# Performance work log

Hardware: AMD Instinct MI355X
Metric: run time of the kernel (lower is better)

Reference implementation:

```python
import jax, jax.numpy as jnp
import numpy as np
from jax import lax

K = 3  # kernel size
KK = K * K


def _bilinear_gather(img, ys, xs):
    """img: [C, H, W]; ys, xs: [KK, H, W] float sample coords.
    Returns [C, KK, H, W], zero outside the image (torch DCN zero-pad semantics)."""
    C, H, W = img.shape
    y0 = jnp.floor(ys).astype(jnp.int32)
    x0 = jnp.floor(xs).astype(jnp.int32)
    y1, x1 = y0 + 1, x0 + 1
    wy1 = ys - y0.astype(ys.dtype)
    wx1 = xs - x0.astype(xs.dtype)
    wy0, wx0 = 1.0 - wy1, 1.0 - wx1

    def g(yi, xi):
        valid = ((yi >= 0) & (yi < H) & (xi >= 0) & (xi < W)).astype(img.dtype)
        yc = jnp.clip(yi, 0, H - 1)
        xc = jnp.clip(xi, 0, W - 1)
        return img[:, yc, xc] * valid[None]  # [C, KK, H, W]

    return (wy0 * wx0) * g(y0, x0) + (wy0 * wx1) * g(y0, x1) \
         + (wy1 * wx0) * g(y1, x0) + (wy1 * wx1) * g(y1, x1)


def _df_layer(x, w_off, b_off, w):
    """One DFConv2d (modulated DCN, k=3, s=1, d=1, pad=1, groups=1) + ReLU."""
    B, C, H, W = x.shape
    O = w.shape[0]
    # offset/mask conv (standard 3x3, pad 1, with bias)
    om = lax.conv_general_dilated(x, w_off, (1, 1), [(1, 1), (1, 1)],
                                  dimension_numbers=('NCHW', 'OIHW', 'NCHW'))
    om = om + b_off[None, :, None, None]                     # [B, 27, H, W]
    off = om[:, :2 * KK].reshape(B, KK, 2, H, W)             # (dy, dx) per kernel pt
    mask = jax.nn.sigmoid(om[:, 2 * KK:3 * KK])              # [B, KK, H, W]

    ki, kj = jnp.meshgrid(jnp.arange(K), jnp.arange(K), indexing='ij')
    # base sampling grid: y = h - pad + i*dil = h + i - 1
    base_y = jnp.arange(H, dtype=x.dtype)[None, :, None] + (ki.reshape(KK, 1, 1).astype(x.dtype) - 1.0)
    base_x = jnp.arange(W, dtype=x.dtype)[None, None, :] + (kj.reshape(KK, 1, 1).astype(x.dtype) - 1.0)
    ys = base_y + off[:, :, 0]                               # [B, KK, H, W]
    xs = base_x + off[:, :, 1]

    sampled = jax.vmap(_bilinear_gather)(x, ys, xs)          # [B, C, KK, H, W]
    out = jnp.einsum('oik,bikhw->bohw', w.reshape(O, C, KK), sampled * mask[:, None])
    return jax.nn.relu(out)


def setup_inputs() -> dict:
    key = jax.random.key(0)
    ks = jax.random.split(key, 7)
    s = 0.05
    return {
        'x': jax.random.normal(ks[0], (2, 256, 96, 96), dtype=jnp.float32),
        'w_off0': jax.random.normal(ks[1], (27, 256, 3, 3), dtype=jnp.float32) * s,
        'b_off0': jnp.zeros((27,), dtype=jnp.float32),
        'w0': jax.random.normal(ks[2], (256, 256, 3, 3), dtype=jnp.float32) * s,
        'w_off1': jax.random.normal(ks[3], (27, 256, 3, 3), dtype=jnp.float32) * s,
        'b_off1': jnp.zeros((27,), dtype=jnp.float32),
        'w1': jax.random.normal(ks[4], (256, 256, 3, 3), dtype=jnp.float32) * s,
    }


def reference(x, w_off0, b_off0, w0, w_off1, b_off1, w1):
    h = _df_layer(x, w_off0, b_off0, w0)
    h = _df_layer(h, w_off1, b_off1, w1)
    return h
```

## Files before the change

### kernel.cpp

```cpp
#include <hip/hip_runtime.h>
#include <cstdint>
#include <cstddef>


#define KTOT 2304
#define PXB  9216

typedef __attribute__((ext_vector_type(8))) short bf16x8;
typedef __attribute__((ext_vector_type(4))) float f32x4;

static __device__ __forceinline__ unsigned short f2bf(float f) {
    union { float f; unsigned int u; } v; v.f = f;
    unsigned int r = (v.u + 0x7FFFu + ((v.u >> 16) & 1u)) >> 16;
    return (unsigned short)r;
}
static __device__ __forceinline__ float bf2f(unsigned short h) {
    union { unsigned int u; float f; } v; v.u = ((unsigned int)h) << 16;
    return v.f;
}
static __device__ __forceinline__ void unpack8(uint4 u, float* f) {
    union { unsigned int u; float f; } t;
    t.u = u.x << 16;         f[0] = t.f;
    t.u = u.x & 0xffff0000u; f[1] = t.f;
    t.u = u.y << 16;         f[2] = t.f;
    t.u = u.y & 0xffff0000u; f[3] = t.f;
    t.u = u.z << 16;         f[4] = t.f;
    t.u = u.z & 0xffff0000u; f[5] = t.f;
    t.u = u.w << 16;         f[6] = t.f;
    t.u = u.w & 0xffff0000u; f[7] = t.f;
}

__global__ __launch_bounds__(256) void transpose_kernel(const float* __restrict__ in,
                                                        unsigned short* __restrict__ outH,
                                                        unsigned short* __restrict__ outL) {
    __shared__ float tile[64][65];
    const int hw0 = blockIdx.x * 64;
    const int c0  = blockIdx.y * 64;
    const int b   = blockIdx.z;
    const int lx  = threadIdx.x & 63;
    const int ly  = threadIdx.x >> 6;
#pragma unroll
    for (int i = 0; i < 16; ++i) {
        int cl = ly + i * 4;
        tile[cl][lx] = in[(size_t)(b * 256 + c0 + cl) * PXB + hw0 + lx];
    }
    __syncthreads();
#pragma unroll
    for (int i = 0; i < 16; ++i) {
        int hwl = ly + i * 4;
        float v = tile[lx][hwl];
        size_t oi = ((size_t)b * PXB + hw0 + hwl) * 256 + c0 + lx;
        unsigned short hi = f2bf(v);
        outH[oi] = hi;
        outL[oi] = f2bf(v - bf2f(hi));
    }
}

__global__ __launch_bounds__(256) void prep_w_kernel(const float* __restrict__ w,
                                                     unsigned short* __restrict__ wA) {
    int idx = blockIdx.x * 256 + threadIdx.x;
    int o = idx / KTOT;
    int k = idx - o * KTOT;
    int kk = k >> 8;
    int c  = k & 255;
    wA[idx] = f2bf(w[o * KTOT + c * 9 + kk]);
}

__global__ __launch_bounds__(256) void prep_woff_kernel(const float* __restrict__ w,
                                                        unsigned short* __restrict__ wH,
                                                        unsigned short* __restrict__ wL) {
    int idx = blockIdx.x * 256 + threadIdx.x;
    int o = idx / KTOT;
    int k = idx - o * KTOT;
    int kk = k >> 8;
    int c  = k & 255;
    float f = (o < 27) ? w[o * KTOT + c * 9 + kk] : 0.0f;
    unsigned short hi = f2bf(f);
    wH[idx] = hi;
    wL[idx] = f2bf(f - bf2f(hi));
}

__global__ __launch_bounds__(512) void offconv_fused(const unsigned short* __restrict__ xH,
                                                     const unsigned short* __restrict__ xL,
                                                     const unsigned short* __restrict__ AH,
                                                     const unsigned short* __restrict__ AL,
                                                     const float* __restrict__ bias,
                                                     float* __restrict__ om) {
    __shared__ __attribute__((aligned(16))) unsigned short AsH[2][32 * 72];
    __shared__ __attribute__((aligned(16))) unsigned short AsL[2][32 * 72];
    __shared__ __attribute__((aligned(16))) unsigned short BsH[2][64 * 72];
    __shared__ __attribute__((aligned(16))) unsigned short BsL[2][64 * 72];

    const int tid  = threadIdx.x;
    const int kg   = tid >> 8;
    const int tl   = tid & 255;
    const int lane = tid & 63;
    const int wq   = (tid >> 6) & 3;
    const int quad = lane >> 4, l16 = lane & 15;
    const int g    = blockIdx.x;
    const int nb   = (g & 7) * 36 + (g >> 3);
    const int n0   = nb * 64;
    const int b    = n0 / PXB;
    const int hw0  = n0 - b * PXB;

    f32x4 acc[2];
#pragma unroll
    for (int mt = 0; mt < 2; ++mt) acc[mt] = (f32x4)0.0f;

    const int arow = tl >> 3, akg = tl & 7;

    uint4 pAH, pAL, pBH0, pBL0, pBH1, pBL1;
    auto pf = [&](int it) {
        const int kt = kg * 18 + it;
        const int kk = kt >> 2, c0 = (kt & 3) * 64;
        const int dy = kk / 3 - 1, dx = kk - (kk / 3) * 3 - 1;
        size_t ai = (size_t)arow * KTOT + kt * 64 + akg * 8;
        pAH = *(const uint4*)&AH[ai];
        pAL = *(const uint4*)&AL[ai];
#pragma unroll
        for (int i = 0; i < 2; ++i) {
            int task = i * 256 + tl;
            int px = task >> 3, cg = task & 7;
            int hw = hw0 + px;
            int h = hw / 96, w = hw - h * 96;
            int y = h + dy, x = w + dx;
            uint4 hv = make_uint4(0u, 0u, 0u, 0u), lv = make_uint4(0u, 0u, 0u, 0u);
            if (((unsigned)y < 96u) && ((unsigned)x < 96u)) {
                size_t bi = ((size_t)b * PXB + y * 96 + x) * 256 + c0 + cg * 8;
                hv = *(const uint4*)&xH[bi];
                lv = *(const uint4*)&xL[bi];
            }
            if (i == 0) { pBH0 = hv; pBL0 = lv; } else { pBH1 = hv; pBL1 = lv; }
        }
    };
    pf(0);

    for (int it = 0; it < 18; ++it) {
        __syncthreads();
        *(uint4*)&AsH[kg][arow * 72 + akg * 8] = pAH;
        *(uint4*)&AsL[kg][arow * 72 + akg * 8] = pAL;
        {
            int px = tl >> 3, cg = tl & 7;
            *(uint4*)&BsH[kg][px * 72 + cg * 8] = pBH0;
            *(uint4*)&BsL[kg][px * 72 + cg * 8] = pBL0;
        }
        {
            int task = 256 + tl;
            int px = task >> 3, cg = task & 7;
            *(uint4*)&BsH[kg][px * 72 + cg * 8] = pBH1;
            *(uint4*)&BsL[kg][px * 72 + cg * 8] = pBL1;
        }
        if (it < 17) pf(it + 1);
        __syncthreads();
#pragma unroll
        for (int ks = 0; ks < 2; ++ks) {
            bf16x8 ah[2], al[2], bh, bl;
#pragma unroll
            for (int mt = 0; mt < 2; ++mt) {
                ah[mt] = *(const bf16x8*)&AsH[kg][(mt * 16 + l16) * 72 + ks * 32 + quad * 8];
                al[mt] = *(const bf16x8*)&AsL[kg][(mt * 16 + l16) * 72 + ks * 32 + quad * 8];
            }
            bh = *(const bf16x8*)&BsH[kg][(wq * 16 + l16) * 72 + ks * 32 + quad * 8];
            bl = *(const bf16x8*)&BsL[kg][(wq * 16 + l16) * 72 + ks * 32 + quad * 8];
#pragma unroll
            for (int mt = 0; mt < 2; ++mt) {
                acc[mt] = __builtin_amdgcn_mfma_f32_16x16x32_bf16(ah[mt], bh, acc[mt], 0, 0, 0);
                acc[mt] = __builtin_amdgcn_mfma_f32_16x16x32_bf16(ah[mt], bl, acc[mt], 0, 0, 0);
                acc[mt] = __builtin_amdgcn_mfma_f32_16x16x32_bf16(al[mt], bh, acc[mt], 0, 0, 0);
            }
        }
    }

    float* red = (float*)BsH;
    __syncthreads();
    if (kg == 1) {
#pragma unroll
        for (int mt = 0; mt < 2; ++mt)
#pragma unroll
            for (int r = 0; r < 4; ++r)
                red[wq * 512 + mt * 256 + quad * 64 + r * 16 + l16] = acc[mt][r];
    }
    __syncthreads();
    if (kg == 0) {
#pragma unroll
        for (int mt = 0; mt < 2; ++mt)
#pragma unroll
            for (int r = 0; r < 4; ++r) {
                float v = acc[mt][r] + red[wq * 512 + mt * 256 + quad * 64 + r * 16 + l16];
                int m = mt * 16 + quad * 4 + r;
                int n = wq * 16 + l16;
                if (m < 27)
                    om[(size_t)(b * 27 + m) * PXB + hw0 + n] = v + bias[m];
            }
    }
}

__global__ __launch_bounds__(512) void dfconv_v6(const unsigned short* __restrict__ xB,
                                                 const float* __restrict__ om,
                                                 const unsigned short* __restrict__ A,
                                                 float* __restrict__ out,
                                                 unsigned short* __restrict__ outH,
                                                 unsigned short* __restrict__ outL,
                                                 int out_mode) {
    __shared__ __attribute__((aligned(16))) char smem[104128];
    unsigned short* BsD  = (unsigned short*)(smem + 65536);
    unsigned short* goff = (unsigned short*)(smem + 88576);
    float*          gwt  = (float*)(smem + 93760);

    const int tid  = threadIdx.x;
    const int wv   = tid >> 6;
    const int lane = tid & 63;
    const int quad = lane >> 4, l16 = lane & 15;
    const int g    = blockIdx.x;
    const int nb   = (g & 7) * 32 + (g >> 3);
    const int b    = nb >> 7;
    const int hw0  = (nb & 127) * 72;

    for (int task = tid; task < 648; task += 512) {
        int px = task / 9;
        int kk = task - px * 9;
        int hw = hw0 + px;
        int h = hw / 96, w = hw - h * 96;
        const float* omp = om + (size_t)b * 27 * PXB + hw;
        float dyv = omp[(size_t)(2 * kk) * PXB];
        float dxv = omp[(size_t)(2 * kk + 1) * PXB];
        float mv  = omp[(size_t)(18 + kk) * PXB];
        float mk  = 1.0f / (1.0f + __expf(-mv));

        float ys = (float)(h + (kk / 3) - 1) + dyv;
        float xs = (float)(w + (kk - (kk / 3) * 3) - 1) + dxv;
        float fy = floorf(ys), fx = floorf(xs);
        int iy = (int)fy, ix = (int)fx;
        float wy1 = ys - fy, wx1 = xs - fx;
        float wy0 = 1.0f - wy1, wx0 = 1.0f - wx1;
        bool yv0 = (unsigned)iy < 96u, yv1 = (unsigned)(iy + 1) < 96u;
        bool xv0 = (unsigned)ix < 96u, xv1 = (unsigned)(ix + 1) < 96u;
        int y0 = min(max(iy, 0), 95),     y1 = min(max(iy + 1, 0), 95);
        int x0 = min(max(ix, 0), 95),     x1 = min(max(ix + 1, 0), 95);
        int gg = task * 4;
        goff[gg + 0] = (unsigned short)(y0 * 96 + x0);
        goff[gg + 1] = (unsigned short)(y0 * 96 + x1);
        goff[gg + 2] = (unsigned short)(y1 * 96 + x0);
        goff[gg + 3] = (unsigned short)(y1 * 96 + x1);
        gwt[gg + 0] = (yv0 && xv0) ? mk * wy0 * wx0 : 0.0f;
        gwt[gg + 1] = (yv0 && xv1) ? mk * wy0 * wx1 : 0.0f;
        gwt[gg + 2] = (yv1 && xv0) ? mk * wy1 * wx0 : 0.0f;
        gwt[gg + 3] = (yv1 && xv1) ? mk * wy1 * wx1 : 0.0f;
    }
    for (int i = tid; i < 576; i += 512) {
        int buf = i / 288, rem = i - buf * 288;
        int row = 72 + rem / 36, col2 = (rem - (rem / 36) * 36) * 2;
        *(unsigned int*)&BsD[buf * 5760 + row * 72 + col2] = 0u;
    }
    __syncthreads();

    const int px  = tid >> 3;
    const int cg  = tid & 7;
    const int px2 = 64 + (tid >> 3);
    const unsigned short* xbase  = xB + (size_t)b * PXB * 256 + cg * 8;

    const int arl = lane >> 3;
    const int akg = (lane & 7) ^ arl;

    f32x4 acc[2][5];
#pragma unroll
    for (int mt = 0; mt < 2; ++mt)
#pragma unroll
        for (int nt = 0; nt < 5; ++nt) acc[mt][nt] = (f32x4)0.0f;

    auto dmaA = [&](int kt, int buf) {
#pragma unroll
        for (int s = 0; s < 4; ++s) {
            const unsigned short* src =
                A + (size_t)(wv * 32 + s * 8 + arl) * KTOT + kt * 64 + akg * 8;
            char* dst = smem + buf * 32768 + wv * 4096 + s * 1024;
            __builtin_amdgcn_global_load_lds(
                (const __attribute__((address_space(1))) unsigned int*)src,
                (__attribute__((address_space(3))) unsigned int*)dst, 16, 0, 0);
        }
    };
    auto loadC = [&](int kt, uint4& c0r, uint4& c1r, uint4& c2r, uint4& c3r,
                     float4& wtr, int pxl) {
        const int tap = kt >> 2, cb0 = (kt & 3) * 64;
        int gg = (pxl * 9 + tap) * 4;
        ushort4 o4 = *(const ushort4*)&goff[gg];
        wtr = *(const float4*)&gwt[gg];
        const unsigned short* cb = xbase + cb0;
        c0r = *(const uint4*)(cb + (size_t)o4.x * 256);
        c1r = *(const uint4*)(cb + (size_t)o4.y * 256);
        c2r = *(const uint4*)(cb + (size_t)o4.z * 256);
        c3r = *(const uint4*)(cb + (size_t)o4.w * 256);
    };
    auto interpC = [&](uint4 c0r, uint4 c1r, uint4 c2r, uint4 c3r, float4 wtr,
                       unsigned short* Bw, int pxl) {
        float f0[8], f1[8], f2[8], f3[8];
        unpack8(c0r, f0); unpack8(c1r, f1); unpack8(c2r, f2); unpack8(c3r, f3);
        unsigned short res[8];
#pragma unroll
        for (int j = 0; j < 8; ++j)
            res[j] = f2bf(wtr.x * f0[j] + wtr.y * f1[j] + wtr.z * f2[j] + wtr.w * f3[j]);
        *(uint4*)&Bw[pxl * 72 + cg * 8] = *(uint4*)res;
    };

    uint4 cc0, cc1, cc2, cc3; float4 cwt;
    uint4 nn0, nn1, nn2, nn3; float4 nwt;
    uint4 dc0, dc1, dc2, dc3; float4 dwt;
    uint4 dn0, dn1, dn2, dn3; float4 dnwt;
    loadC(0, cc0, cc1, cc2, cc3, cwt, px);
    if (tid < 64) loadC(0, dc0, dc1, dc2, dc3, dwt, px2);
    loadC(1, nn0, nn1, nn2, nn3, nwt, px);
    if (tid < 64) loadC(1, dn0, dn1, dn2, dn3, dnwt, px2);
    dmaA(0, 0);
    __builtin_amdgcn_sched_barrier(0);
    if (wv == 0) { asm volatile("s_waitcnt vmcnt(12)" ::: "memory"); }
    else         { asm volatile("s_waitcnt vmcnt(8)"  ::: "memory"); }
    __builtin_amdgcn_sched_barrier(0);
    interpC(cc0, cc1, cc2, cc3, cwt, BsD, px);
    if (tid < 64) interpC(dc0, dc1, dc2, dc3, dwt, BsD, px2);
    cc0 = nn0; cc1 = nn1; cc2 = nn2; cc3 = nn3; cwt = nwt;
    if (tid < 64) { dc0 = dn0; dc1 = dn1; dc2 = dn2; dc3 = dn3; dwt = dnwt; }
    asm volatile("s_waitcnt lgkmcnt(0)" ::: "memory");
    __builtin_amdgcn_sched_barrier(0);
    __builtin_amdgcn_s_barrier();

    for (int r = 0; r < 36; ++r) {
        const int cur = r & 1;

        if (r <= 33) {
            loadC(r + 2, nn0, nn1, nn2, nn3, nwt, px);
            if (tid < 64) loadC(r + 2, dn0, dn1, dn2, dn3, dnwt, px2);
        }
        if (r <= 34) dmaA(r + 1, cur ^ 1);

        __builtin_amdgcn_sched_barrier(0);
        if (r <= 33) {
            if (wv == 0) { asm volatile("s_waitcnt vmcnt(12)" ::: "memory"); }
            else         { asm volatile("s_waitcnt vmcnt(8)"  ::: "memory"); }
        } else if (r == 34) {
            asm volatile("s_waitcnt vmcnt(4)" ::: "memory");
        } else {
            asm volatile("s_waitcnt vmcnt(0)" ::: "memory");
        }
        __builtin_amdgcn_sched_barrier(0);

        {
            const char* Ac = smem + cur * 32768 + wv * 4096;
            const int sw0 = ((quad ^ (l16 & 7)) * 16);
            const int sw1 = (((4 + quad) ^ (l16 & 7)) * 16);
            bf16x8 af00 = *(const bf16x8*)(Ac + l16 * 128 + sw0);
            bf16x8 af01 = *(const bf16x8*)(Ac + (16 + l16) * 128 + sw0);
            bf16x8 af10 = *(const bf16x8*)(Ac + l16 * 128 + sw1);
            bf16x8 af11 = *(const bf16x8*)(Ac + (16 + l16) * 128 + sw1);
            const unsigned short* Br = BsD + cur * 5760;
#pragma unroll
            for (int nt = 0; nt < 5; ++nt) {
                bf16x8 b0 = *(const bf16x8*)&Br[(nt * 16 + l16) * 72 + quad * 8];
                acc[0][nt] = __builtin_amdgcn_mfma_f32_16x16x32_bf16(af00, b0, acc[0][nt], 0, 0, 0);
                acc[1][nt] = __builtin_amdgcn_mfma_f32_16x16x32_bf16(af01, b0, acc[1][nt], 0, 0, 0);
            }
#pragma unroll
            for (int nt = 0; nt < 5; ++nt) {
                bf16x8 b1 = *(const bf16x8*)&Br[(nt * 16 + l16) * 72 + 32 + quad * 8];
                acc[0][nt] = __builtin_amdgcn_mfma_f32_16x16x32_bf16(af10, b1, acc[0][nt], 0, 0, 0);
                acc[1][nt] = __builtin_amdgcn_mfma_f32_16x16x32_bf16(af11, b1, acc[1][nt], 0, 0, 0);
            }
        }

        if (r <= 34) {
            unsigned short* Bw = BsD + (cur ^ 1) * 5760;
            interpC(cc0, cc1, cc2, cc3, cwt, Bw, px);
            if (tid < 64) interpC(dc0, dc1, dc2, dc3, dwt, Bw, px2);
            cc0 = nn0; cc1 = nn1; cc2 = nn2; cc3 = nn3; cwt = nwt;
            if (tid < 64) { dc0 = dn0; dc1 = dn1; dc2 = dn2; dc3 = dn3; dwt = dnwt; }
        }

        asm volatile("s_waitcnt lgkmcnt(0)" ::: "memory");
        __builtin_amdgcn_sched_barrier(0);
        __builtin_amdgcn_s_barrier();
    }

    asm volatile("s_waitcnt vmcnt(0) lgkmcnt(0)" ::: "memory");
    __syncthreads();

    float* tileS = (float*)smem;
    if (out_mode == 0) {
#pragma unroll
        for (int pass = 0; pass < 4; ++pass) {
            if ((wv >> 1) == pass) {
#pragma unroll
                for (int mt = 0; mt < 2; ++mt)
#pragma unroll
                    for (int nt = 0; nt < 5; ++nt)
#pragma unroll
                        for (int rr = 0; rr < 4; ++rr) {
                            int ml = (wv & 1) * 32 + mt * 16 + quad * 4 + rr;
                            int n  = nt * 16 + l16;
                            tileS[ml * 80 + n] = fmaxf(acc[mt][nt][rr], 0.0f);
                        }
            }
            __syncthreads();
#pragma unroll
            for (int j = 0; j < 3; ++j) {
                int idx = j * 512 + tid;
                if (idx < 1152) {
                    int row = idx / 18, q = idx - row * 18;
                    *(float4*)&out[(size_t)(b * 256 + pass * 64 + row) * PXB + hw0 + q * 4] =
                        *(const float4*)&tileS[row * 80 + q * 4];
                }
            }
            __syncthreads();
        }
    } else {
#pragma unroll
        for (int pass = 0; pass < 5; ++pass) {
#pragma unroll
            for (int mt = 0; mt < 2; ++mt) {
                f32x4 v = acc[mt][pass];
                v[0] = fmaxf(v[0], 0.f); v[1] = fmaxf(v[1], 0.f);
                v[2] = fmaxf(v[2], 0.f); v[3] = fmaxf(v[3], 0.f);
                *(f32x4*)&tileS[l16 * 264 + wv * 32 + mt * 16 + quad * 4] = v;
            }
            __syncthreads();
            const int cnt = (pass < 4) ? 1024 : 512;
#pragma unroll
            for (int j = 0; j < 2; ++j) {
                int idx = j * 512 + tid;
                if (idx < cnt) {
                    int pxl = idx >> 6, ln = idx & 63;
                    float4 v = *(const float4*)&tileS[pxl * 264 + ln * 4];
                    size_t oi = ((size_t)b * PXB + hw0 + pass * 16 + pxl) * 256 + ln * 4;
                    unsigned short hv[4], lv[4];
#pragma unroll
                    for (int e = 0; e < 4; ++e) {
                        float fe = (e == 0) ? v.x : (e == 1) ? v.y : (e == 2) ? v.z : v.w;
                        hv[e] = f2bf(fe);
                        lv[e] = f2bf(fe - bf2f(hv[e]));
                    }
                    *(ushort4*)&outH[oi] = *(ushort4*)hv;
                    *(ushort4*)&outL[oi] = *(ushort4*)lv;
                }
            }
            __syncthreads();
        }
    }
}

extern "C" void kernel_launch(void* const* d_in, const int* in_sizes, int n_in,
                              void* d_out, int out_size, void* d_ws, size_t ws_size,
                              hipStream_t stream) {
    const float* x     = (const float*)d_in[0];
    const float* woff0 = (const float*)d_in[1];
    const float* boff0 = (const float*)d_in[2];
    const float* w0    = (const float*)d_in[3];
    const float* woff1 = (const float*)d_in[4];
    const float* boff1 = (const float*)d_in[5];
    const float* w1    = (const float*)d_in[6];
    float* out = (float*)d_out;

    char* p = (char*)d_ws;
    float* om  = (float*)p;  p += (size_t)2 * 27 * PXB * 4;
    unsigned short* xh  = (unsigned short*)p; p += (size_t)2 * 256 * PXB * 2;
    unsigned short* xl  = (unsigned short*)p; p += (size_t)2 * 256 * PXB * 2;
    unsigned short* h1h = (unsigned short*)p; p += (size_t)2 * 256 * PXB * 2;
    unsigned short* h1l = (unsigned short*)p; p += (size_t)2 * 256 * PXB * 2;
    unsigned short* wA0 = (unsigned short*)p; p += (size_t)256 * KTOT * 2;
    unsigned short* wA1 = (unsigned short*)p; p += (size_t)256 * KTOT * 2;
    unsigned short* wH0 = (unsigned short*)p; p += (size_t)32 * KTOT * 2;
    unsigned short* wL0 = (unsigned short*)p; p += (size_t)32 * KTOT * 2;
    unsigned short* wH1 = (unsigned short*)p; p += (size_t)32 * KTOT * 2;
    unsigned short* wL1 = (unsigned short*)p; p += (size_t)32 * KTOT * 2;

    hipLaunchKernelGGL(transpose_kernel, dim3(PXB / 64, 4, 2), dim3(256), 0, stream, x, xh, xl);
    hipLaunchKernelGGL(prep_w_kernel, dim3(256 * KTOT / 256), dim3(256), 0, stream, w0, wA0);
    hipLaunchKernelGGL(prep_w_kernel, dim3(256 * KTOT / 256), dim3(256), 0, stream, w1, wA1);
    hipLaunchKernelGGL(prep_woff_kernel, dim3(32 * KTOT / 256), dim3(256), 0, stream, woff0, wH0, wL0);
    hipLaunchKernelGGL(prep_woff_kernel, dim3(32 * KTOT / 256), dim3(256), 0, stream, woff1, wH1, wL1);

    hipLaunchKernelGGL(offconv_fused, dim3(288), dim3(512), 0, stream, xh, xl, wH0, wL0, boff0, om);
    hipLaunchKernelGGL(dfconv_v6, dim3(256), dim3(512), 0, stream, xh, om, wA0,
                       (float*)nullptr, h1h, h1l, 1);

    hipLaunchKernelGGL(offconv_fused, dim3(288), dim3(512), 0, stream, h1h, h1l, wH1, wL1, boff1, om);
    hipLaunchKernelGGL(dfconv_v6, dim3(256), dim3(512), 0, stream, h1h, om, wA1,
                       out, (unsigned short*)nullptr, (unsigned short*)nullptr, 0);
}
```

Before: 258.1 us.

## Double-buffer shared memory in offset conv with two-stage register prefetch

Rewrites the offset/mask convolution kernel to use double-buffered LDS tiles with a two-iteration-deep global prefetch. Each iteration now needs only one barrier instead of two, and the LDS store for the next tile overlaps the MFMA compute on the current tile. The cost is doubled LDS use, about 110KB per block, and more live registers, which may reduce occupancy. The custom waitcnt and sched_barrier also need careful ordering to stay correct.

```diff
diff --git a/kernel.cpp b/kernel.cpp
--- a/kernel.cpp
+++ b/kernel.cpp
@@ -80,16 +80,16 @@
     wL[idx] = f2bf(f - bf2f(hi));
 }
 
-__global__ __launch_bounds__(512) void offconv_fused(const unsigned short* __restrict__ xH,
-                                                     const unsigned short* __restrict__ xL,
-                                                     const unsigned short* __restrict__ AH,
-                                                     const unsigned short* __restrict__ AL,
-                                                     const float* __restrict__ bias,
-                                                     float* __restrict__ om) {
-    __shared__ __attribute__((aligned(16))) unsigned short AsH[2][32 * 72];
-    __shared__ __attribute__((aligned(16))) unsigned short AsL[2][32 * 72];
-    __shared__ __attribute__((aligned(16))) unsigned short BsH[2][64 * 72];
-    __shared__ __attribute__((aligned(16))) unsigned short BsL[2][64 * 72];
+__global__ __launch_bounds__(512) void offconv_v2(const unsigned short* __restrict__ xH,
+                                                  const unsigned short* __restrict__ xL,
+                                                  const unsigned short* __restrict__ AH,
+                                                  const unsigned short* __restrict__ AL,
+                                                  const float* __restrict__ bias,
+                                                  float* __restrict__ om) {
+    __shared__ __attribute__((aligned(16))) unsigned short AsH[2 * 2 * 32 * 72];
+    __shared__ __attribute__((aligned(16))) unsigned short AsL[2 * 2 * 32 * 72];
+    __shared__ __attribute__((aligned(16))) unsigned short BsH[2 * 2 * 64 * 72];
+    __shared__ __attribute__((aligned(16))) unsigned short BsL[2 * 2 * 64 * 72];
 
     const int tid  = threadIdx.x;
     const int kg   = tid >> 8;
@@ -108,67 +108,101 @@
     for (int mt = 0; mt < 2; ++mt) acc[mt] = (f32x4)0.0f;
 
     const int arow = tl >> 3, akg = tl & 7;
-
-    uint4 pAH, pAL, pBH0, pBL0, pBH1, pBL1;
-    auto pf = [&](int it) {
+    const int px0 = tl >> 3,          cg0 = tl & 7;
+    const int px1 = (256 + tl) >> 3,  cg1 = tl & 7;
+
+    auto pfL = [&](int it, uint4& rAH, uint4& rAL, uint4& rB0H, uint4& rB0L,
+                   uint4& rB1H, uint4& rB1L) {
         const int kt = kg * 18 + it;
         const int kk = kt >> 2, c0 = (kt & 3) * 64;
         const int dy = kk / 3 - 1, dx = kk - (kk / 3) * 3 - 1;
         size_t ai = (size_t)arow * KTOT + kt * 64 + akg * 8;
-        pAH = *(const uint4*)&AH[ai];
-        pAL = *(const uint4*)&AL[ai];
-#pragma unroll
-        for (int i = 0; i < 2; ++i) {
-            int task = i * 256 + tl;
-            int px = task >> 3, cg = task & 7;
-            int hw = hw0 + px;
+        rAH = *(const uint4*)&AH[ai];
+        rAL = *(const uint4*)&AL[ai];
+        {
+            int hw = hw0 + px0;
             int h = hw / 96, w = hw - h * 96;
             int y = h + dy, x = w + dx;
-            uint4 hv = make_uint4(0u, 0u, 0u, 0u), lv = make_uint4(0u, 0u, 0u, 0u);
+            uint4 hv = make_uint4(0u, 0u, 0u, 0u), lv = hv;
             if (((unsigned)y < 96u) && ((unsigned)x < 96u)) {
-                size_t bi = ((size_t)b * PXB + y * 96 + x) * 256 + c0 + cg * 8;
+                size_t bi = ((size_t)b * PXB + y * 96 + x) * 256 + c0 + cg0 * 8;
                 hv = *(const uint4*)&xH[bi];
                 lv = *(const uint4*)&xL[bi];
             }
-            if (i == 0) { pBH0 = hv; pBL0 = lv; } else { pBH1 = hv; pBL1 = lv; }
+            rB0H = hv; rB0L = lv;
+        }
+        {
+            int hw = hw0 + px1;
+            int h = hw / 96, w = hw - h * 96;
+            int y = h + dy, x = w + dx;
+            uint4 hv = make_uint4(0u, 0u, 0u, 0u), lv = hv;
+            if (((unsigned)y < 96u) && ((unsigned)x < 96u)) {
+                size_t bi = ((size_t)b * PXB + y * 96 + x) * 256 + c0 + cg1 * 8;
+                hv = *(const uint4*)&xH[bi];
+                lv = *(const uint4*)&xL[bi];
+            }
+            rB1H = hv; rB1L = lv;
         }
     };
-    pf(0);
+    auto writeSet = [&](int db, uint4 sAH, uint4 sAL, uint4 sB0H, uint4 sB0L,
+                        uint4 sB1H, uint4 sB1L) {
+        const int ab = (db * 2 + kg) * 2304;
+        const int bb = (db * 2 + kg) * 4608;
+        *(uint4*)&AsH[ab + arow * 72 + akg * 8] = sAH;
+        *(uint4*)&AsL[ab + arow * 72 + akg * 8] = sAL;
+        *(uint4*)&BsH[bb + px0 * 72 + cg0 * 8] = sB0H;
+        *(uint4*)&BsL[bb + px0 * 72 + cg0 * 8] = sB0L;
+        *(uint4*)&BsH[bb + px1 * 72 + cg1 * 8] = sB1H;
+        *(uint4*)&BsL[bb + px1 * 72 + cg1 * 8] = sB1L;
+    };
+
+    uint4 cAH, cAL, cB0H, cB0L, cB1H, cB1L;
+    uint4 nAH, nAL, nB0H, nB0L, nB1H, nB1L;
+
+    pfL(0, cAH, cAL, cB0H, cB0L, cB1H, cB1L);
+    pfL(1, nAH, nAL, nB0H, nB0L, nB1H, nB1L);
+    writeSet(0, cAH, cAL, cB0H, cB0L, cB1H, cB1L);
+    cAH = nAH; cAL = nAL; cB0H = nB0H; cB0L = nB0L; cB1H = nB1H; cB1L = nB1L;
+    asm volatile("s_waitcnt lgkmcnt(0)" ::: "memory");
+    __builtin_amdgcn_sched_barrier(0);
+    __builtin_amdgcn_s_barrier();
 
     for (int it = 0; it < 18; ++it) {
-        __syncthreads();
-        *(uint4*)&AsH[kg][arow * 72 + akg * 8] = pAH;
-        *(uint4*)&AsL[kg][arow * 72 + akg * 8] = pAL;
+        const int db = it & 1;
+
+        if (it <= 15)
+            pfL(it + 2, nAH, nAL, nB0H, nB0L, nB1H, nB1L);
+
+        if (it <= 16)
+            writeSet(db ^ 1, cAH, cAL, cB0H, cB0L, cB1H, cB1L);
+
         {
-            int px = tl >> 3, cg = tl & 7;
-            *(uint4*)&BsH[kg][px * 72 + cg * 8] = pBH0;
-            *(uint4*)&BsL[kg][px * 72 + cg * 8] = pBL0;
-        }
-        {
-            int task = 256 + tl;
-            int px = task >> 3, cg = task & 7;
-            *(uint4*)&BsH[kg][px * 72 + cg * 8] = pBH1;
-            *(uint4*)&BsL[kg][px * 72 + cg * 8] = pBL1;
-        }
-        if (it < 17) pf(it + 1);
-        __syncthreads();
-#pragma unroll
-        for (int ks = 0; ks < 2; ++ks) {
-            bf16x8 ah[2], al[2], bh, bl;
-#pragma unroll
-            for (int mt = 0; mt < 2; ++mt) {
-                ah[mt] = *(const bf16x8*)&AsH[kg][(mt * 16 + l16) * 72 + ks * 32 + quad * 8];
-                al[mt] = *(const bf16x8*)&AsL[kg][(mt * 16 + l16) * 72 + ks * 32 + quad * 8];
-            }
-            bh = *(const bf16x8*)&BsH[kg][(wq * 16 + l16) * 72 + ks * 32 + quad * 8];
-            bl = *(const bf16x8*)&BsL[kg][(wq * 16 + l16) * 72 + ks * 32 + quad * 8];
-#pragma unroll
-            for (int mt = 0; mt < 2; ++mt) {
-                acc[mt] = __builtin_amdgcn_mfma_f32_16x16x32_bf16(ah[mt], bh, acc[mt], 0, 0, 0);
-                acc[mt] = __builtin_amdgcn_mfma_f32_16x16x32_bf16(ah[mt], bl, acc[mt], 0, 0, 0);
-                acc[mt] = __builtin_amdgcn_mfma_f32_16x16x32_bf16(al[mt], bh, acc[mt], 0, 0, 0);
-            }
-        }
+            const int ab = (db * 2 + kg) * 2304;
+            const int bb = (db * 2 + kg) * 4608;
+#pragma unroll
+            for (int ks = 0; ks < 2; ++ks) {
+                bf16x8 ah[2], al[2], bh, bl;
+#pragma unroll
+                for (int mt = 0; mt < 2; ++mt) {
+                    ah[mt] = *(const bf16x8*)&AsH[ab + (mt * 16 + l16) * 72 + ks * 32 + quad * 8];
+                    al[mt] = *(const bf16x8*)&AsL[ab + (mt * 16 + l16) * 72 + ks * 32 + quad * 8];
+                }
+                bh = *(const bf16x8*)&BsH[bb + (wq * 16 + l16) * 72 + ks * 32 + quad * 8];
+                bl = *(const bf16x8*)&BsL[bb + (wq * 16 + l16) * 72 + ks * 32 + quad * 8];
+#pragma unroll
+                for (int mt = 0; mt < 2; ++mt) {
+                    acc[mt] = __builtin_amdgcn_mfma_f32_16x16x32_bf16(ah[mt], bh, acc[mt], 0, 0, 0);
+                    acc[mt] = __builtin_amdgcn_mfma_f32_16x16x32_bf16(ah[mt], bl, acc[mt], 0, 0, 0);
+                    acc[mt] = __builtin_amdgcn_mfma_f32_16x16x32_bf16(al[mt], bh, acc[mt], 0, 0, 0);
+                }
+            }
+        }
+
+        cAH = nAH; cAL = nAL; cB0H = nB0H; cB0L = nB0L; cB1H = nB1H; cB1L = nB1L;
+
+        asm volatile("s_waitcnt lgkmcnt(0)" ::: "memory");
+        __builtin_amdgcn_sched_barrier(0);
+        __builtin_amdgcn_s_barrier();
     }
 
     float* red = (float*)BsH;
@@ -476,11 +510,11 @@
     hipLaunchKernelGGL(prep_woff_kernel, dim3(32 * KTOT / 256), dim3(256), 0, stream, woff0, wH0, wL0);
     hipLaunchKernelGGL(prep_woff_kernel, dim3(32 * KTOT / 256), dim3(256), 0, stream, woff1, wH1, wL1);
 
-    hipLaunchKernelGGL(offconv_fused, dim3(288), dim3(512), 0, stream, xh, xl, wH0, wL0, boff0, om);
+    hipLaunchKernelGGL(offconv_v2, dim3(288), dim3(512), 0, stream, xh, xl, wH0, wL0, boff0, om);
     hipLaunchKernelGGL(dfconv_v6, dim3(256), dim3(512), 0, stream, xh, om, wA0,
                        (float*)nullptr, h1h, h1l, 1);
 
-    hipLaunchKernelGGL(offconv_fused, dim3(288), dim3(512), 0, stream, h1h, h1l, wH1, wL1, boff1, om);
+    hipLaunchKernelGGL(offconv_v2, dim3(288), dim3(512), 0, stream, h1h, h1l, wH1, wL1, boff1, om);
     hipLaunchKernelGGL(dfconv_v6, dim3(256), dim3(512), 0, stream, h1h, om, wA1,
                        out, (unsigned short*)nullptr, (unsigned short*)nullptr, 0);
 }
```

Result: slower. 284.9 us (+10.4%).

## Restructure offset conv into smaller double-buffered tiles with register prefetch

Applied to the files above, without the earlier changes.

The offset/mask conv kernel now uses 256-thread blocks over 32-pixel tiles, launched as 576 blocks instead of 288. The old intra-block split-K with an LDS reduction is gone. The K loop runs all 36 steps with a double-buffered LDS ring and a two-stage register prefetch, so only one barrier is needed per step. This aims to raise occupancy and overlap global loads with MFMA, but each A tile is now loaded twice as often across blocks and each wave has less MFMA work per barrier.

```diff
diff --git a/kernel.cpp b/kernel.cpp
--- a/kernel.cpp
+++ b/kernel.cpp
@@ -80,7 +80,7 @@
     wL[idx] = f2bf(f - bf2f(hi));
 }
 
-__global__ __launch_bounds__(512) void offconv_fused(const unsigned short* __restrict__ xH,
+__global__ __launch_bounds__(256, 4) void offconv_v3(const unsigned short* __restrict__ xH,
                                                      const unsigned short* __restrict__ xL,
                                                      const unsigned short* __restrict__ AH,
                                                      const unsigned short* __restrict__ AL,
@@ -88,110 +88,94 @@
                                                      float* __restrict__ om) {
     __shared__ __attribute__((aligned(16))) unsigned short AsH[2][32 * 72];
     __shared__ __attribute__((aligned(16))) unsigned short AsL[2][32 * 72];
-    __shared__ __attribute__((aligned(16))) unsigned short BsH[2][64 * 72];
-    __shared__ __attribute__((aligned(16))) unsigned short BsL[2][64 * 72];
+    __shared__ __attribute__((aligned(16))) unsigned short BsH[2][32 * 72];
+    __shared__ __attribute__((aligned(16))) unsigned short BsL[2][32 * 72];
 
     const int tid  = threadIdx.x;
-    const int kg   = tid >> 8;
-    const int tl   = tid & 255;
+    const int wv   = tid >> 6;
     const int lane = tid & 63;
-    const int wq   = (tid >> 6) & 3;
     const int quad = lane >> 4, l16 = lane & 15;
+    const int mt   = wv & 1;
+    const int nt   = wv >> 1;
     const int g    = blockIdx.x;
-    const int nb   = (g & 7) * 36 + (g >> 3);
-    const int n0   = nb * 64;
+    const int nb   = (g & 7) * 72 + (g >> 3);
+    const int n0   = nb * 32;
     const int b    = n0 / PXB;
     const int hw0  = n0 - b * PXB;
 
-    f32x4 acc[2];
-#pragma unroll
-    for (int mt = 0; mt < 2; ++mt) acc[mt] = (f32x4)0.0f;
-
-    const int arow = tl >> 3, akg = tl & 7;
-
-    uint4 pAH, pAL, pBH0, pBL0, pBH1, pBL1;
-    auto pf = [&](int it) {
-        const int kt = kg * 18 + it;
+    const int arow = tid >> 3, acol = tid & 7;
+    const int px   = tid >> 3, cg   = tid & 7;
+
+    f32x4 acc = (f32x4)0.0f;
+
+    auto pfL = [&](int kt, uint4& rAH, uint4& rAL, uint4& rBH, uint4& rBL) {
         const int kk = kt >> 2, c0 = (kt & 3) * 64;
         const int dy = kk / 3 - 1, dx = kk - (kk / 3) * 3 - 1;
-        size_t ai = (size_t)arow * KTOT + kt * 64 + akg * 8;
-        pAH = *(const uint4*)&AH[ai];
-        pAL = *(const uint4*)&AL[ai];
-#pragma unroll
-        for (int i = 0; i < 2; ++i) {
-            int task = i * 256 + tl;
-            int px = task >> 3, cg = task & 7;
-            int hw = hw0 + px;
-            int h = hw / 96, w = hw - h * 96;
-            int y = h + dy, x = w + dx;
-            uint4 hv = make_uint4(0u, 0u, 0u, 0u), lv = make_uint4(0u, 0u, 0u, 0u);
-            if (((unsigned)y < 96u) && ((unsigned)x < 96u)) {
-                size_t bi = ((size_t)b * PXB + y * 96 + x) * 256 + c0 + cg * 8;
-                hv = *(const uint4*)&xH[bi];
-                lv = *(const uint4*)&xL[bi];
-            }
-            if (i == 0) { pBH0 = hv; pBL0 = lv; } else { pBH1 = hv; pBL1 = lv; }
-        }
+        size_t ai = (size_t)arow * KTOT + kt * 64 + acol * 8;
+        rAH = *(const uint4*)&AH[ai];
+        rAL = *(const uint4*)&AL[ai];
+        int hw = hw0 + px;
+        int h = hw / 96, w = hw - h * 96;
+        int y = h + dy, x = w + dx;
+        uint4 hv = make_uint4(0u, 0u, 0u, 0u), lv = hv;
+        if (((unsigned)y < 96u) && ((unsigned)x < 96u)) {
+            size_t bi = ((size_t)b * PXB + y * 96 + x) * 256 + c0 + cg * 8;
+            hv = *(const uint4*)&xH[bi];
+            lv = *(const uint4*)&xL[bi];
+        }
+        rBH = hv; rBL = lv;
     };
-    pf(0);
-
-    for (int it = 0; it < 18; ++it) {
-        __syncthreads();
-        *(uint4*)&AsH[kg][arow * 72 + akg * 8] = pAH;
-        *(uint4*)&AsL[kg][arow * 72 + akg * 8] = pAL;
-        {
-            int px = tl >> 3, cg = tl & 7;
-            *(uint4*)&BsH[kg][px * 72 + cg * 8] = pBH0;
-            *(uint4*)&BsL[kg][px * 72 + cg * 8] = pBL0;
-        }
-        {
-            int task = 256 + tl;
-            int px = task >> 3, cg = task & 7;
-            *(uint4*)&BsH[kg][px * 72 + cg * 8] = pBH1;
-            *(uint4*)&BsL[kg][px * 72 + cg * 8] = pBL1;
-        }
-        if (it < 17) pf(it + 1);
-        __syncthreads();
+    auto writeSet = [&](int db, uint4 sAH, uint4 sAL, uint4 sBH, uint4 sBL) {
+        *(uint4*)&AsH[db][arow * 72 + acol * 8] = sAH;
+        *(uint4*)&AsL[db][arow * 72 + acol * 8] = sAL;
+        *(uint4*)&BsH[db][px * 72 + cg * 8]     = sBH;
+        *(uint4*)&BsL[db][px * 72 + cg * 8]     = sBL;
+    };
+
+    uint4 cAH, cAL, cBH, cBL;
+    uint4 nAH, nAL, nBH, nBL;
+
+    pfL(0, cAH, cAL, cBH, cBL);
+    pfL(1, nAH, nAL, nBH, nBL);
+    writeSet(0, cAH, cAL, cBH, cBL);
+    cAH = nAH; cAL = nAL; cBH = nBH; cBL = nBL;
+    asm volatile("s_waitcnt lgkmcnt(0)" ::: "memory");
+    __builtin_amdgcn_sched_barrier(0);
+    __builtin_amdgcn_s_barrier();
+
+    for (int r = 0; r < 36; ++r) {
+        const int db = r & 1;
+
+        if (r <= 33)
+            pfL(r + 2, nAH, nAL, nBH, nBL);
+
+        if (r <= 34)
+            writeSet(db ^ 1, cAH, cAL, cBH, cBL);
+
 #pragma unroll
         for (int ks = 0; ks < 2; ++ks) {
-            bf16x8 ah[2], al[2], bh, bl;
-#pragma unroll
-            for (int mt = 0; mt < 2; ++mt) {
-                ah[mt] = *(const bf16x8*)&AsH[kg][(mt * 16 + l16) * 72 + ks * 32 + quad * 8];
-                al[mt] = *(const bf16x8*)&AsL[kg][(mt * 16 + l16) * 72 + ks * 32 + quad * 8];
-            }
-            bh = *(const bf16x8*)&BsH[kg][(wq * 16 + l16) * 72 + ks * 32 + quad * 8];
-            bl = *(const bf16x8*)&BsL[kg][(wq * 16 + l16) * 72 + ks * 32 + quad * 8];
-#pragma unroll
-            for (int mt = 0; mt < 2; ++mt) {
-                acc[mt] = __builtin_amdgcn_mfma_f32_16x16x32_bf16(ah[mt], bh, acc[mt], 0, 0, 0);
-                acc[mt] = __builtin_amdgcn_mfma_f32_16x16x32_bf16(ah[mt], bl, acc[mt], 0, 0, 0);
-                acc[mt] = __builtin_amdgcn_mfma_f32_16x16x32_bf16(al[mt], bh, acc[mt], 0, 0, 0);
-            }
-        }
-    }
-
-    float* red = (float*)BsH;
-    __syncthreads();
-    if (kg == 1) {
-#pragma unroll
-        for (int mt = 0; mt < 2; ++mt)
-#pragma unroll
-            for (int r = 0; r < 4; ++r)
-                red[wq * 512 + mt * 256 + quad * 64 + r * 16 + l16] = acc[mt][r];
-    }
-    __syncthreads();
-    if (kg == 0) {
-#pragma unroll
-        for (int mt = 0; mt < 2; ++mt)
-#pragma unroll
-            for (int r = 0; r < 4; ++r) {
-                float v = acc[mt][r] + red[wq * 512 + mt * 256 + quad * 64 + r * 16 + l16];
-                int m = mt * 16 + quad * 4 + r;
-                int n = wq * 16 + l16;
-                if (m < 27)
-                    om[(size_t)(b * 27 + m) * PXB + hw0 + n] = v + bias[m];
-            }
+            bf16x8 ah = *(const bf16x8*)&AsH[db][(mt * 16 + l16) * 72 + ks * 32 + quad * 8];
+            bf16x8 al = *(const bf16x8*)&AsL[db][(mt * 16 + l16) * 72 + ks * 32 + quad * 8];
+            bf16x8 bh = *(const bf16x8*)&BsH[db][(nt * 16 + l16) * 72 + ks * 32 + quad * 8];
+            bf16x8 bl = *(const bf16x8*)&BsL[db][(nt * 16 + l16) * 72 + ks * 32 + quad * 8];
+            acc = __builtin_amdgcn_mfma_f32_16x16x32_bf16(ah, bh, acc, 0, 0, 0);
+            acc = __builtin_amdgcn_mfma_f32_16x16x32_bf16(ah, bl, acc, 0, 0, 0);
+            acc = __builtin_amdgcn_mfma_f32_16x16x32_bf16(al, bh, acc, 0, 0, 0);
+        }
+
+        cAH = nAH; cAL = nAL; cBH = nBH; cBL = nBL;
+
+        asm volatile("s_waitcnt lgkmcnt(0)" ::: "memory");
+        __builtin_amdgcn_sched_barrier(0);
+        __builtin_amdgcn_s_barrier();
+    }
+
+#pragma unroll
+    for (int rr = 0; rr < 4; ++rr) {
+        int m = mt * 16 + quad * 4 + rr;
+        int n = nt * 16 + l16;
+        if (m < 27)
+            om[(size_t)(b * 27 + m) * PXB + hw0 + n] = acc[rr] + bias[m];
     }
 }
 
@@ -476,11 +460,11 @@
     hipLaunchKernelGGL(prep_woff_kernel, dim3(32 * KTOT / 256), dim3(256), 0, stream, woff0, wH0, wL0);
     hipLaunchKernelGGL(prep_woff_kernel, dim3(32 * KTOT / 256), dim3(256), 0, stream, woff1, wH1, wL1);
 
-    hipLaunchKernelGGL(offconv_fused, dim3(288), dim3(512), 0, stream, xh, xl, wH0, wL0, boff0, om);
+    hipLaunchKernelGGL(offconv_v3, dim3(576), dim3(256), 0, stream, xh, xl, wH0, wL0, boff0, om);
     hipLaunchKernelGGL(dfconv_v6, dim3(256), dim3(512), 0, stream, xh, om, wA0,
                        (float*)nullptr, h1h, h1l, 1);
 
-    hipLaunchKernelGGL(offconv_fused, dim3(288), dim3(512), 0, stream, h1h, h1l, wH1, wL1, boff1, om);
+    hipLaunchKernelGGL(offconv_v3, dim3(576), dim3(256), 0, stream, h1h, h1l, wH1, wL1, boff1, om);
     hipLaunchKernelGGL(dfconv_v6, dim3(256), dim3(512), 0, stream, h1h, om, wA1,
                        out, (unsigned short*)nullptr, (unsigned short*)nullptr, 0);
 }
```

New measurement: 255.6 us. Within noise of the previous version (-0.9%).
